# Kernel optimization log

Measured on AMD Instinct MI355X. Metric: run time of the kernel, lower is better.

The kernel has to match this reference:

```python
import jax, jax.numpy as jnp
import numpy as np

B, T, H, NH = 4, 2048, 1024, 16
HD = H // NH  # 64


def setup_inputs() -> dict:
    key = jax.random.key(0)
    ks = jax.random.split(key, 8)
    s = 1.0 / np.sqrt(H)
    return {
        "hidden_states": jax.random.normal(ks[0], (B, T, H), dtype=jnp.float32),
        "attention_mask": jnp.zeros((B, 1, 1, T), dtype=jnp.float32),
        "Wq": jax.random.normal(ks[1], (H, H), dtype=jnp.float32) * s,
        "bq": jax.random.normal(ks[2], (H,), dtype=jnp.float32) * 0.01,
        "Wk": jax.random.normal(ks[3], (H, H), dtype=jnp.float32) * s,
        "bk": jax.random.normal(ks[4], (H,), dtype=jnp.float32) * 0.01,
        "Wv": jax.random.normal(ks[5], (H, H), dtype=jnp.float32) * s,
        "bv": jax.random.normal(ks[6], (H,), dtype=jnp.float32) * 0.01,
    }


def _split_heads(x):
    # [b, t, h*d] -> [b, h, t, d]
    b, t, _ = x.shape
    return x.reshape(b, t, NH, HD).transpose(0, 2, 1, 3)


def reference(hidden_states, attention_mask, Wq, bq, Wk, bk, Wv, bv):
    q = _split_heads(hidden_states @ Wq.T + bq)
    k = _split_heads(hidden_states @ Wk.T + bk)
    v = _split_heads(hidden_states @ Wv.T + bv)
    scores = jnp.einsum('bhqd,bhkd->bhqk', q, k) / jnp.sqrt(jnp.float32(HD))
    t = q.shape[2]
    causal = jnp.triu(jnp.ones((t, t), dtype=scores.dtype), k=1)[None, None] * (-1e9)
    scores = scores + causal + attention_mask
    probs = jax.nn.softmax(scores, axis=-1)
    # module returns [b, h, t, d] (no merge back)
    return jnp.einsum('bhqk,bhkd->bhqd', probs, v)
```

## Files before the change

kernel.cpp:

```cpp
#include <hip/hip_runtime.h>
#include <hip/hip_bf16.h>


typedef float  f32x4 __attribute__((ext_vector_type(4)));
typedef short  s16x8 __attribute__((ext_vector_type(8)));
typedef unsigned short u16;

#define LOG2E 1.44269504088896340736f

__device__ __forceinline__ u16 f2bf(float f) {
  unsigned u = __float_as_uint(f);
  u += 0x7FFFu + ((u >> 16) & 1u);
  return (u16)(u >> 16);
}
__device__ __forceinline__ float bf2f(u16 v) {
  return __uint_as_float(((unsigned)v) << 16);
}
__device__ __forceinline__ float ex2(float x) {
#if __has_builtin(__builtin_amdgcn_exp2f)
  return __builtin_amdgcn_exp2f(x);
#else
  return exp2f(x);
#endif
}
__device__ __forceinline__ float rcp_(float x) {
#if __has_builtin(__builtin_amdgcn_rcpf)
  return __builtin_amdgcn_rcpf(x);
#else
  return 1.0f / x;
#endif
}
__device__ __forceinline__ unsigned cvtpk(float lo, float hi) {
  unsigned r;
  asm("v_cvt_pk_bf16_f32 %0, %1, %2" : "=v"(r) : "v"(lo), "v"(hi));
  return r;
}
__device__ __forceinline__ void bar() {
  asm volatile("" ::: "memory");
  __builtin_amdgcn_s_barrier();
  asm volatile("" ::: "memory");
}

#define GLOAD16(gp, lp)                                                          \
  __builtin_amdgcn_global_load_lds(                                              \
      (const __attribute__((address_space(1))) void*)(gp),                       \
      (__attribute__((address_space(3))) void*)(lp), 16, 0, 0)

#define MFMA(a, b, c) __builtin_amdgcn_mfma_f32_16x16x32_bf16((a), (b), (c), 0, 0, 0)

__global__ __launch_bounds__(256) void cvt_all(
    const float* __restrict__ hs, const float* __restrict__ wq,
    const float* __restrict__ wk, const float* __restrict__ wv,
    const float* __restrict__ maskp,
    u16* __restrict__ xo, u16* __restrict__ qo, u16* __restrict__ ko,
    u16* __restrict__ vo, u16* __restrict__ wm) {
  int b = blockIdx.x;
  const float* s;
  u16* d;
  size_t i;
  bool isw = false;
  if (b < 4096) { s = hs; d = xo; i = (size_t)b * 256 + threadIdx.x; }
  else if (b < 5632) {
    int w = (b - 4096) >> 9, r = (b - 4096) & 511;
    s = (w == 0) ? wq : (w == 1) ? wk : wv;
    d = (w == 0) ? qo : (w == 1) ? ko : vo;
    i = (size_t)r * 256 + threadIdx.x;
  } else {
    s = maskp; d = wm; i = (size_t)(b - 5632) * 256 + threadIdx.x;
    isw = true;
  }
  const float4* sp = (const float4*)s + i * 2;
  float4 a = sp[0], c = sp[1];
  s16x8 r8;
  if (isw) {
    r8[0] = f2bf(ex2(a.x * LOG2E)); r8[1] = f2bf(ex2(a.y * LOG2E));
    r8[2] = f2bf(ex2(a.z * LOG2E)); r8[3] = f2bf(ex2(a.w * LOG2E));
    r8[4] = f2bf(ex2(c.x * LOG2E)); r8[5] = f2bf(ex2(c.y * LOG2E));
    r8[6] = f2bf(ex2(c.z * LOG2E)); r8[7] = f2bf(ex2(c.w * LOG2E));
  } else {
    r8[0] = f2bf(a.x); r8[1] = f2bf(a.y); r8[2] = f2bf(a.z); r8[3] = f2bf(a.w);
    r8[4] = f2bf(c.x); r8[5] = f2bf(c.y); r8[6] = f2bf(c.z); r8[7] = f2bf(c.w);
  }
  *(s16x8*)(d + i * 8) = r8;
}

__global__ __launch_bounds__(512, 2) void qkv_gemm(
    const u16* __restrict__ Xb,
    const u16* __restrict__ Wqb, const u16* __restrict__ Wkb,
    const u16* __restrict__ Wvb,
    const float* __restrict__ bq, const float* __restrict__ bk,
    const float* __restrict__ bv, const u16* __restrict__ Wm,
    u16* __restrict__ Qo, u16* __restrict__ Ko, u16* __restrict__ Vto) {
  int bid0 = blockIdx.x;
  int bid  = (bid0 & 7) * 96 + (bid0 >> 3);
  int which = bid % 3;
  int rt = bid / 3;
  int mt = rt >> 3, nt = rt & 7;
  const u16* W = (which == 0) ? Wqb : (which == 1) ? Wkb : Wvb;
  const float* bias = (which == 0) ? bq : (which == 1) ? bk : bv;

  __shared__ __align__(16) char lds[98304];

  int tid = threadIdx.x;
  int lane = tid & 63, wid = tid >> 6;
  int q16 = lane & 15, g = lane >> 4;
  int wr = wid >> 1, wc = wid & 1;

  int srow = tid >> 3, sslot = tid & 7;
  int sw = (sslot ^ (srow & 7)) << 4;
  const char* Asrc = (const char*)Xb + (size_t)(mt * 256 + srow) * 2048 + sw;
  const char* Bsrc = (const char*)W  + (size_t)(nt * 128 + srow) * 2048 + sw;

  int slot0 = (g ^ (q16 & 7)) << 4;

#define STAGE_AB(tt, buf) do { size_t so = (size_t)(tt) * 128;                   \
    GLOAD16(Asrc + so,          lds + (buf) * 32768 + tid * 16);                 \
    GLOAD16(Asrc + so + 131072, lds + (buf) * 32768 + 8192 + tid * 16);          \
    GLOAD16(Asrc + so + 262144, lds + (buf) * 32768 + 16384 + tid * 16);         \
    GLOAD16(Asrc + so + 393216, lds + (buf) * 32768 + 24576 + tid * 16);         \
    GLOAD16(Bsrc + so,          lds + 65536 + (buf) * 16384 + tid * 16);         \
    GLOAD16(Bsrc + so + 131072, lds + 65536 + (buf) * 16384 + 8192 + tid * 16); } while (0)

#define LDA(FA, buf, mp) do {                                                    \
    const char* p_ = lds + (buf) * 32768 + (wr * 64 + (mp) * 32 + q16) * 128;    \
    FA[0] = *(const s16x8*)(p_ + slot0);                                         \
    FA[1] = *(const s16x8*)(p_ + (slot0 ^ 64));                                  \
    FA[2] = *(const s16x8*)(p_ + 2048 + slot0);                                  \
    FA[3] = *(const s16x8*)(p_ + 2048 + (slot0 ^ 64)); } while (0)

#define LDB(FB, buf) do {                                                        \
    const char* p_ = lds + 65536 + (buf) * 16384 + (wc * 64 + q16) * 128;        \
    FB[0] = *(const s16x8*)(p_ + slot0);                                         \
    FB[1] = *(const s16x8*)(p_ + (slot0 ^ 64));                                  \
    FB[2] = *(const s16x8*)(p_ + 2048 + slot0);                                  \
    FB[3] = *(const s16x8*)(p_ + 2048 + (slot0 ^ 64));                           \
    FB[4] = *(const s16x8*)(p_ + 4096 + slot0);                                  \
    FB[5] = *(const s16x8*)(p_ + 4096 + (slot0 ^ 64));                           \
    FB[6] = *(const s16x8*)(p_ + 6144 + slot0);                                  \
    FB[7] = *(const s16x8*)(p_ + 6144 + (slot0 ^ 64)); } while (0)

#define MM16(mlo, FA, FB) do {                                                   \
    _Pragma("unroll")                                                            \
    for (int n_ = 0; n_ < 4; ++n_) {                                             \
      acc[(mlo)][n_]     = MFMA(FA[0], FB[2 * n_],     acc[(mlo)][n_]);          \
      acc[(mlo)][n_]     = MFMA(FA[1], FB[2 * n_ + 1], acc[(mlo)][n_]);          \
      acc[(mlo) + 1][n_] = MFMA(FA[2], FB[2 * n_],     acc[(mlo) + 1][n_]);      \
      acc[(mlo) + 1][n_] = MFMA(FA[3], FB[2 * n_ + 1], acc[(mlo) + 1][n_]);      \
    } } while (0)

  STAGE_AB(0, 0);

  f32x4 acc[4][4] = {};
  s16x8 fA0[4], fA1[4], fB[8];

#pragma unroll 1
  for (int i = 0; i < 16; ++i) {
    int buf = i & 1;
    if (i < 15) {
      STAGE_AB(i + 1, buf ^ 1);
      asm volatile("s_waitcnt vmcnt(6)" ::: "memory");
    } else {
      asm volatile("s_waitcnt vmcnt(0)" ::: "memory");
    }
    bar();
    LDA(fA0, buf, 0);
    LDA(fA1, buf, 1);
    LDB(fB, buf);
    __builtin_amdgcn_s_setprio(1);
    MM16(0, fA0, fB);
    MM16(2, fA1, fB);
    __builtin_amdgcn_s_setprio(0);
    bar();
  }

  u16* tile = (u16*)(void*)lds + (size_t)wid * 64 * 72;
  int h0 = nt * 2 + wc;
  int m_base = mt * 256 + wr * 64;
  int bb = m_base >> 11;
  int t0 = m_base & 2047;

  if (which != 2) {
    float qsc = (which == 0) ? (0.125f * LOG2E) : 1.0f;
#pragma unroll
    for (int n = 0; n < 4; ++n) {
      float bvl = bias[h0 * 64 + n * 16 + q16];
#pragma unroll
      for (int m = 0; m < 4; ++m)
#pragma unroll
        for (int j = 0; j < 4; ++j)
          tile[(m * 16 + g * 4 + j) * 72 + n * 16 + q16] =
              f2bf((acc[m][n][j] + bvl) * qsc);
    }
  } else {
    const u16* wrow = Wm + (size_t)bb * 2048 + t0;
    float wv[4][4];
#pragma unroll
    for (int m = 0; m < 4; ++m)
#pragma unroll
      for (int j = 0; j < 4; ++j)
        wv[m][j] = bf2f(wrow[m * 16 + g * 4 + j]);
#pragma unroll
    for (int n = 0; n < 4; ++n) {
      float bvl = bias[h0 * 64 + n * 16 + q16];
#pragma unroll
      for (int m = 0; m < 4; ++m)
#pragma unroll
        for (int j = 0; j < 4; ++j)
          tile[(n * 16 + q16) * 72 + m * 16 + g * 4 + j] =
              f2bf((acc[m][n][j] + bvl) * wv[m][j]);
    }
  }
  asm volatile("" ::: "memory");

  const char* tb = (const char*)tile;
  int rl = lane >> 3, cb = (lane & 7) * 16;
  if (which != 2) {
    u16* Out = (which == 0) ? Qo : Ko;
    char* gbase = (char*)(Out + ((size_t)(bb * 16 + h0) * 2048 + t0) * 64);
#pragma unroll
    for (int c = 0; c < 8; ++c) {
      int row = rl + c * 8;
      s16x8 v = *(const s16x8*)(tb + row * 144 + cb);
      *(s16x8*)(gbase + row * 128 + cb) = v;
    }
  } else {
    char* gbase = (char*)Vto + ((size_t)(bb * 16 + h0) * 64) * 4096 + t0 * 2;
#pragma unroll
    for (int c = 0; c < 8; ++c) {
      int d = rl + c * 8;
      s16x8 v = *(const s16x8*)(tb + d * 144 + cb);
      *(s16x8*)(gbase + (size_t)d * 4096 + cb) = v;
    }
  }
#undef STAGE_AB
#undef LDA
#undef LDB
#undef MM16
}

__global__ __launch_bounds__(256, 4) void attn_fwd(
    const u16* __restrict__ Qw, const u16* __restrict__ Kw,
    const u16* __restrict__ Vtw, const u16* __restrict__ Wm,
    float* __restrict__ out) {
  int bid0 = blockIdx.x;
  int bid = (bid0 & 7) * 128 + (bid0 >> 3);
  int bh = bid >> 4, qt = bid & 15;
  int qb = qt << 7;
  int tid = threadIdx.x;
  int lane = tid & 63, wid = tid >> 6;
  int q16 = lane & 15, g = lane >> 4;

  __shared__ __align__(16) char Ks[2][8192];
  __shared__ __align__(16) char Vs[2][8192];
  __shared__ __align__(16) u16 wl[2048];

  int qw0 = qb + wid * 32;
  size_t qr = (size_t)bh * 2048 + qw0 + q16;
  s16x8 qa00 = *(const s16x8*)(Qw + qr * 64 + g * 8);
  s16x8 qa01 = *(const s16x8*)(Qw + qr * 64 + 32 + g * 8);
  s16x8 qa10 = *(const s16x8*)(Qw + (qr + 16) * 64 + g * 8);
  s16x8 qa11 = *(const s16x8*)(Qw + (qr + 16) * 64 + 32 + g * 8);

  int srow = tid >> 3;
  int sinner = (tid & 7) << 4;
  int fs = (srow & 7) ^ ((srow >> 1) & 4);
  int ssw = sinner ^ (fs << 4);
  const char* Kg = (const char*)Kw + ((size_t)bh * 2048 + srow) * 128 + ssw;
  const char* Vg = (const char*)Vtw + ((size_t)bh * 64 + srow) * 4096 + ssw;

  GLOAD16((const char*)Wm + (size_t)(bh >> 4) * 4096 + tid * 16,
          (char*)wl + tid * 16);
  GLOAD16(Kg, Ks[0] + tid * 16);
  GLOAD16(Kg + 4096, Ks[0] + tid * 16 + 4096);
  GLOAD16(Vg, Vs[0] + tid * 16);
  GLOAD16(Vg + 131072, Vs[0] + tid * 16 + 4096);
  __syncthreads();

  f32x4 o0[4] = {}, o1[4] = {};
  f32x4 lw0 = {}, lw1 = {};

  int qc0 = qw0 + q16, qc1 = qc0 + 16;
  int ntile = 2 * qt + 2;

  for (int kt = 0; kt < ntile; ++kt) {
    int cur = kt & 1;
    if (kt + 1 < ntile) {
      size_t kb2 = (size_t)(kt + 1) << 6;
      char* kd = Ks[cur ^ 1] + tid * 16;
      char* vd = Vs[cur ^ 1] + tid * 16;
      GLOAD16(Kg + kb2 * 128, kd);
      GLOAD16(Kg + kb2 * 128 + 4096, kd + 4096);
      GLOAD16(Vg + kb2 * 2, vd);
      GLOAD16(Vg + kb2 * 2 + 131072, vd + 4096);
      asm volatile("s_waitcnt vmcnt(4)" ::: "memory");
    } else {
      asm volatile("s_waitcnt vmcnt(0)" ::: "memory");
    }
    __builtin_amdgcn_s_barrier();
    asm volatile("" ::: "memory");

    int kb = kt << 6;
    const char* ksb = Ks[cur];
    const char* vsb = Vs[cur];

    if (64 * kt <= qw0 + 31) {
      bool causal = (64 * kt + 63 > qw0);
#pragma unroll
      for (int c = 0; c < 2; ++c) {
        f32x4 sA0[2], sA1[2];
        __builtin_amdgcn_s_setprio(1);
#pragma unroll
        for (int t4 = 0; t4 < 2; ++t4) {
          int kk = 32 * c + ((q16 >> 2) << 3) + (t4 << 2) + (q16 & 3);
          int fk = (kk & 7) ^ ((kk >> 1) & 4);
          const char* krow = ksb + kk * 128;
          int in0 = (g * 16) ^ (fk << 4);
          s16x8 kf0 = *(const s16x8*)(krow + in0);
          s16x8 kf1 = *(const s16x8*)(krow + (in0 ^ 64));
          f32x4 sv = {0.f, 0.f, 0.f, 0.f};
          sv = MFMA(kf0, qa00, sv);
          sv = MFMA(kf1, qa01, sv);
          sA0[t4] = sv;
          f32x4 su = {0.f, 0.f, 0.f, 0.f};
          su = MFMA(kf0, qa10, su);
          su = MFMA(kf1, qa11, su);
          sA1[t4] = su;
        }
        __builtin_amdgcn_s_setprio(0);

        s16x8 wf = *(const s16x8*)((const char*)wl + (kb + 32 * c + 8 * g) * 2);

        union { s16x8 v; unsigned u[4]; } pb0, pb1;
#pragma unroll
        for (int t4 = 0; t4 < 2; ++t4) {
          float a0 = ex2(sA0[t4][0]), a1 = ex2(sA0[t4][1]);
          float a2 = ex2(sA0[t4][2]), a3 = ex2(sA0[t4][3]);
          float b0 = ex2(sA1[t4][0]), b1 = ex2(sA1[t4][1]);
          float b2 = ex2(sA1[t4][2]), b3 = ex2(sA1[t4][3]);
          if (causal) {
            int k0 = kb + 32 * c + 8 * g + 4 * t4;
            a0 = (k0 + 0 <= qc0) ? a0 : 0.f;
            a1 = (k0 + 1 <= qc0) ? a1 : 0.f;
            a2 = (k0 + 2 <= qc0) ? a2 : 0.f;
            a3 = (k0 + 3 <= qc0) ? a3 : 0.f;
            b0 = (k0 + 0 <= qc1) ? b0 : 0.f;
            b1 = (k0 + 1 <= qc1) ? b1 : 0.f;
            b2 = (k0 + 2 <= qc1) ? b2 : 0.f;
            b3 = (k0 + 3 <= qc1) ? b3 : 0.f;
          }
          pb0.u[t4 * 2 + 0] = cvtpk(a0, a1);
          pb0.u[t4 * 2 + 1] = cvtpk(a2, a3);
          pb1.u[t4 * 2 + 0] = cvtpk(b0, b1);
          pb1.u[t4 * 2 + 1] = cvtpk(b2, b3);
        }

        __builtin_amdgcn_s_setprio(1);
#pragma unroll
        for (int dt = 0; dt < 4; ++dt) {
          int d = dt * 16 + q16;
          int fv = (d & 7) ^ ((d >> 1) & 4);
          s16x8 vf = *(const s16x8*)(vsb + d * 128 + ((64 * c + 16 * g) ^ (fv << 4)));
          o0[dt] = MFMA(vf, pb0.v, o0[dt]);
          o1[dt] = MFMA(vf, pb1.v, o1[dt]);
        }
        lw0 = MFMA(wf, pb0.v, lw0);
        lw1 = MFMA(wf, pb1.v, lw1);
        __builtin_amdgcn_s_setprio(0);
      }
    }
    __builtin_amdgcn_s_barrier();
  }

  float i0 = rcp_(lw0[0]), i1 = rcp_(lw1[0]);
  float* op0 = out + ((size_t)bh * 2048 + qc0) * 64 + g * 4;
  float* op1 = out + ((size_t)bh * 2048 + qc1) * 64 + g * 4;
#pragma unroll
  for (int dt = 0; dt < 4; ++dt) {
    *(f32x4*)(op0 + dt * 16) = o0[dt] * i0;
    *(f32x4*)(op1 + dt * 16) = o1[dt] * i1;
  }
}

extern "C" void kernel_launch(void* const* d_in, const int* in_sizes, int n_in,
                              void* d_out, int out_size, void* d_ws, size_t ws_size,
                              hipStream_t stream) {
  const float* hs   = (const float*)d_in[0];
  const float* mask = (const float*)d_in[1];
  const float* Wq   = (const float*)d_in[2];
  const float* bq   = (const float*)d_in[3];
  const float* Wk   = (const float*)d_in[4];
  const float* bk   = (const float*)d_in[5];
  const float* Wv   = (const float*)d_in[6];
  const float* bv   = (const float*)d_in[7];
  float* out = (float*)d_out;

  char* w = (char*)d_ws;
  u16* Xb  = (u16*)w; w += (size_t)8192 * 1024 * 2;
  u16* Wqb = (u16*)w; w += (size_t)1024 * 1024 * 2;
  u16* Wkb = (u16*)w; w += (size_t)1024 * 1024 * 2;
  u16* Wvb = (u16*)w; w += (size_t)1024 * 1024 * 2;
  u16* Qw  = (u16*)w; w += (size_t)8192 * 1024 * 2;
  u16* Kw  = (u16*)w; w += (size_t)8192 * 1024 * 2;
  u16* Vtw = (u16*)w; w += (size_t)8192 * 1024 * 2;
  u16* Wm  = (u16*)w; w += (size_t)8192 * 2;

  cvt_all<<<5636, 256, 0, stream>>>(hs, Wq, Wk, Wv, mask, Xb, Wqb, Wkb, Wvb, Wm);
  qkv_gemm<<<768, 512, 0, stream>>>(Xb, Wqb, Wkb, Wvb, bq, bk, bv, Wm, Qw, Kw, Vtw);
  attn_fwd<<<1024, 256, 0, stream>>>(Qw, Kw, Vtw, Wm, out);
}
```

Baseline: 142.0 us.

## Double attention query tile to 256 rows per block with balanced causal scheduling

```diff
diff --git a/kernel.cpp b/kernel.cpp
--- a/kernel.cpp
+++ b/kernel.cpp
@@ -238,14 +238,16 @@
 #undef MM16
 }
 
-__global__ __launch_bounds__(256, 4) void attn_fwd(
+__global__ __launch_bounds__(256, 2) void attn_fwd(
     const u16* __restrict__ Qw, const u16* __restrict__ Kw,
     const u16* __restrict__ Vtw, const u16* __restrict__ Wm,
     float* __restrict__ out) {
   int bid0 = blockIdx.x;
-  int bid = (bid0 & 7) * 128 + (bid0 >> 3);
-  int bh = bid >> 4, qt = bid & 15;
-  int qb = qt << 7;
+  int x = bid0 & 7, kk0 = bid0 >> 3;
+  int r = kk0 >> 5, cc = kk0 & 31, u = cc & 7;
+  int qt = r ? 7 - u : u;
+  int bh = x * 8 + ((cc >> 3) | (r << 2));
+  int qb = qt << 8;
   int tid = threadIdx.x;
   int lane = tid & 63, wid = tid >> 6;
   int q16 = lane & 15, g = lane >> 4;
@@ -254,12 +256,14 @@
   __shared__ __align__(16) char Vs[2][8192];
   __shared__ __align__(16) u16 wl[2048];
 
-  int qw0 = qb + wid * 32;
+  int qw0 = qb + wid * 64;
   size_t qr = (size_t)bh * 2048 + qw0 + q16;
-  s16x8 qa00 = *(const s16x8*)(Qw + qr * 64 + g * 8);
-  s16x8 qa01 = *(const s16x8*)(Qw + qr * 64 + 32 + g * 8);
-  s16x8 qa10 = *(const s16x8*)(Qw + (qr + 16) * 64 + g * 8);
-  s16x8 qa11 = *(const s16x8*)(Qw + (qr + 16) * 64 + 32 + g * 8);
+  s16x8 qa[4][2];
+#pragma unroll
+  for (int h = 0; h < 4; ++h) {
+    qa[h][0] = *(const s16x8*)(Qw + (qr + 16 * h) * 64 + g * 8);
+    qa[h][1] = *(const s16x8*)(Qw + (qr + 16 * h) * 64 + 32 + g * 8);
+  }
 
   int srow = tid >> 3;
   int sinner = (tid & 7) << 4;
@@ -276,11 +280,10 @@
   GLOAD16(Vg + 131072, Vs[0] + tid * 16 + 4096);
   __syncthreads();
 
-  f32x4 o0[4] = {}, o1[4] = {};
-  f32x4 lw0 = {}, lw1 = {};
-
-  int qc0 = qw0 + q16, qc1 = qc0 + 16;
-  int ntile = 2 * qt + 2;
+  f32x4 o[4][4] = {};
+  f32x4 lw[4] = {};
+
+  int ntile = 4 * qt + 4;
 
   for (int kt = 0; kt < ntile; ++kt) {
     int cur = kt & 1;
@@ -303,11 +306,11 @@
     const char* ksb = Ks[cur];
     const char* vsb = Vs[cur];
 
-    if (64 * kt <= qw0 + 31) {
+    if (64 * kt <= qw0 + 63) {
       bool causal = (64 * kt + 63 > qw0);
 #pragma unroll
       for (int c = 0; c < 2; ++c) {
-        f32x4 sA0[2], sA1[2];
+        f32x4 sA[2][4];
         __builtin_amdgcn_s_setprio(1);
 #pragma unroll
         for (int t4 = 0; t4 < 2; ++t4) {
@@ -317,41 +320,36 @@
           int in0 = (g * 16) ^ (fk << 4);
           s16x8 kf0 = *(const s16x8*)(krow + in0);
           s16x8 kf1 = *(const s16x8*)(krow + (in0 ^ 64));
-          f32x4 sv = {0.f, 0.f, 0.f, 0.f};
-          sv = MFMA(kf0, qa00, sv);
-          sv = MFMA(kf1, qa01, sv);
-          sA0[t4] = sv;
-          f32x4 su = {0.f, 0.f, 0.f, 0.f};
-          su = MFMA(kf0, qa10, su);
-          su = MFMA(kf1, qa11, su);
-          sA1[t4] = su;
+#pragma unroll
+          for (int h = 0; h < 4; ++h) {
+            f32x4 sv = {0.f, 0.f, 0.f, 0.f};
+            sv = MFMA(kf0, qa[h][0], sv);
+            sv = MFMA(kf1, qa[h][1], sv);
+            sA[t4][h] = sv;
+          }
         }
         __builtin_amdgcn_s_setprio(0);
 
         s16x8 wf = *(const s16x8*)((const char*)wl + (kb + 32 * c + 8 * g) * 2);
 
-        union { s16x8 v; unsigned u[4]; } pb0, pb1;
-#pragma unroll
-        for (int t4 = 0; t4 < 2; ++t4) {
-          float a0 = ex2(sA0[t4][0]), a1 = ex2(sA0[t4][1]);
-          float a2 = ex2(sA0[t4][2]), a3 = ex2(sA0[t4][3]);
-          float b0 = ex2(sA1[t4][0]), b1 = ex2(sA1[t4][1]);
-          float b2 = ex2(sA1[t4][2]), b3 = ex2(sA1[t4][3]);
-          if (causal) {
-            int k0 = kb + 32 * c + 8 * g + 4 * t4;
-            a0 = (k0 + 0 <= qc0) ? a0 : 0.f;
-            a1 = (k0 + 1 <= qc0) ? a1 : 0.f;
-            a2 = (k0 + 2 <= qc0) ? a2 : 0.f;
-            a3 = (k0 + 3 <= qc0) ? a3 : 0.f;
-            b0 = (k0 + 0 <= qc1) ? b0 : 0.f;
-            b1 = (k0 + 1 <= qc1) ? b1 : 0.f;
-            b2 = (k0 + 2 <= qc1) ? b2 : 0.f;
-            b3 = (k0 + 3 <= qc1) ? b3 : 0.f;
+        union { s16x8 v; unsigned u[4]; } pb[4];
+#pragma unroll
+        for (int h = 0; h < 4; ++h) {
+          int qc = qw0 + 16 * h + q16;
+#pragma unroll
+          for (int t4 = 0; t4 < 2; ++t4) {
+            float a0 = ex2(sA[t4][h][0]), a1 = ex2(sA[t4][h][1]);
+            float a2 = ex2(sA[t4][h][2]), a3 = ex2(sA[t4][h][3]);
+            if (causal) {
+              int k0 = kb + 32 * c + 8 * g + 4 * t4;
+              a0 = (k0 + 0 <= qc) ? a0 : 0.f;
+              a1 = (k0 + 1 <= qc) ? a1 : 0.f;
+              a2 = (k0 + 2 <= qc) ? a2 : 0.f;
+              a3 = (k0 + 3 <= qc) ? a3 : 0.f;
+            }
+            pb[h].u[t4 * 2 + 0] = cvtpk(a0, a1);
+            pb[h].u[t4 * 2 + 1] = cvtpk(a2, a3);
           }
-          pb0.u[t4 * 2 + 0] = cvtpk(a0, a1);
-          pb0.u[t4 * 2 + 1] = cvtpk(a2, a3);
-          pb1.u[t4 * 2 + 0] = cvtpk(b0, b1);
-          pb1.u[t4 * 2 + 1] = cvtpk(b2, b3);
         }
 
         __builtin_amdgcn_s_setprio(1);
@@ -360,24 +358,26 @@
           int d = dt * 16 + q16;
           int fv = (d & 7) ^ ((d >> 1) & 4);
           s16x8 vf = *(const s16x8*)(vsb + d * 128 + ((64 * c + 16 * g) ^ (fv << 4)));
-          o0[dt] = MFMA(vf, pb0.v, o0[dt]);
-          o1[dt] = MFMA(vf, pb1.v, o1[dt]);
+#pragma unroll
+          for (int h = 0; h < 4; ++h)
+            o[h][dt] = MFMA(vf, pb[h].v, o[h][dt]);
         }
-        lw0 = MFMA(wf, pb0.v, lw0);
-        lw1 = MFMA(wf, pb1.v, lw1);
+#pragma unroll
+        for (int h = 0; h < 4; ++h)
+          lw[h] = MFMA(wf, pb[h].v, lw[h]);
         __builtin_amdgcn_s_setprio(0);
       }
     }
     __builtin_amdgcn_s_barrier();
   }
 
-  float i0 = rcp_(lw0[0]), i1 = rcp_(lw1[0]);
-  float* op0 = out + ((size_t)bh * 2048 + qc0) * 64 + g * 4;
-  float* op1 = out + ((size_t)bh * 2048 + qc1) * 64 + g * 4;
-#pragma unroll
-  for (int dt = 0; dt < 4; ++dt) {
-    *(f32x4*)(op0 + dt * 16) = o0[dt] * i0;
-    *(f32x4*)(op1 + dt * 16) = o1[dt] * i1;
+#pragma unroll
+  for (int h = 0; h < 4; ++h) {
+    float inv = rcp_(lw[h][0]);
+    float* op = out + ((size_t)bh * 2048 + qw0 + 16 * h + q16) * 64 + g * 4;
+#pragma unroll
+    for (int dt = 0; dt < 4; ++dt)
+      *(f32x4*)(op + dt * 16) = o[h][dt] * inv;
   }
 }
 
@@ -406,5 +406,5 @@
 
   cvt_all<<<5636, 256, 0, stream>>>(hs, Wq, Wk, Wv, mask, Xb, Wqb, Wkb, Wvb, Wm);
   qkv_gemm<<<768, 512, 0, stream>>>(Xb, Wqb, Wkb, Wvb, bq, bk, bv, Wm, Qw, Kw, Vtw);
-  attn_fwd<<<1024, 256, 0, stream>>>(Qw, Kw, Vtw, Wm, out);
-}
+  attn_fwd<<<512, 256, 0, stream>>>(Qw, Kw, Vtw, Wm, out);
+}
```

Result: slower. 147.3 us (+3.7%).
